# Optimization experiments

Measured on AMD Instinct MI355X. Metric: run time of the kernel, lower is better.

Reference implementation:

```python
import jax, jax.numpy as jnp
import numpy as np

N_NODES = 30000
E_EDGES = 480000
IN_DIM = 256
REL_DIM = 128
OUT_DIM = 512


def setup_inputs() -> dict:
    key = jax.random.key(0)
    ks = jax.random.split(key, 12)
    h = jax.random.normal(ks[0], (N_NODES, IN_DIM), dtype=jnp.float32)
    node_att = jax.random.uniform(ks[1], (N_NODES, 1), dtype=jnp.float32)
    rel = jax.random.normal(ks[2], (E_EDGES, REL_DIM), dtype=jnp.float32)
    edge_att = jax.random.uniform(ks[3], (E_EDGES, 1), dtype=jnp.float32)
    src = jax.random.randint(ks[4], (E_EDGES,), 0, N_NODES, dtype=jnp.int32)
    dst = jax.random.randint(ks[5], (E_EDGES,), 0, N_NODES, dtype=jnp.int32)
    # learned params (Linear: y = x @ W + b), scaled like default torch init
    def lin(k, fan_in, fan_out):
        k1, k2 = jax.random.split(k)
        bound = 1.0 / np.sqrt(fan_in)
        W = jax.random.uniform(k1, (fan_in, fan_out), minval=-bound, maxval=bound, dtype=jnp.float32)
        b = jax.random.uniform(k2, (fan_out,), minval=-bound, maxval=bound, dtype=jnp.float32)
        return W, b
    Wn, bn = lin(ks[6], IN_DIM, IN_DIM)
    Wr, br = lin(ks[7], REL_DIM, REL_DIM)
    Wa, ba = lin(ks[8], 2 * IN_DIM + REL_DIM, OUT_DIM)
    return {"h": h, "node_att": node_att, "rel": rel, "edge_att": edge_att,
            "Wn": Wn, "bn": bn, "Wr": Wr, "br": br, "Wa": Wa, "ba": ba,
            "src": src, "dst": dst}


def reference(h, node_att, rel, edge_att, Wn, bn, Wr, br, Wa, ba, src, dst):
    n_nodes = h.shape[0]
    # apply_nodes: h <- node_fc(h)  (runs BEFORE message passing)
    h2 = h @ Wn + bn                                   # [N, in]
    # message: z1 = att_src*h_src + att_dst*h_dst      [E, in]
    z1 = node_att[src] * h2[src] + node_att[dst] * h2[dst]
    # z2 = edge_att * rel_fc(rel)                      [E, rel]
    z2 = edge_att * (rel @ Wr + br)
    msg = jnp.concatenate([z1, z2], axis=1)            # [E, in+rel]
    # reduce: sum messages into destination nodes
    h_sum = jax.ops.segment_sum(msg, dst, num_segments=n_nodes)  # [N, in+rel]
    # apply_fc + relu on cat([h, h_sum])               [N, 2*in+rel] -> [N, out]
    out = jax.nn.relu(jnp.concatenate([h2, h_sum], axis=1) @ Wa + ba)
    return out
```

## Files before the change

kernel.cpp:

```cpp
#include <hip/hip_runtime.h>

#define E_EDGES 480000
#define N_NODES 30000
#define IN_DIM 256
#define REL_DIM 128
#define OUT_DIM 512
#define CAT_DIM 640
#define MTILES 1875

typedef float f32x4 __attribute__((ext_vector_type(4)));
typedef __bf16 bf16x8 __attribute__((ext_vector_type(8)));
typedef unsigned short u16x8 __attribute__((ext_vector_type(8)));

static __device__ __forceinline__ unsigned short f2bf(float x) {
    union { float f; unsigned int u; } c; c.f = x;
    unsigned int u = c.u;
    unsigned int r = u + 0x7fffu + ((u >> 16) & 1u);
    return (unsigned short)(r >> 16);
}
static __device__ __forceinline__ float bf2f(unsigned short b) {
    union { unsigned int u; float f; } c; c.u = ((unsigned int)b) << 16;
    return c.f;
}

__global__ void k_count(const int* __restrict__ dst, int* __restrict__ cnt) {
    int e = blockIdx.x * 256 + threadIdx.x;
    if (e < E_EDGES) atomicAdd(&cnt[dst[e]], 1);
}

__global__ void k_scan(const int* __restrict__ cnt, int* __restrict__ off,
                       int* __restrict__ cur) {
    __shared__ int part[1024];
    const int t = threadIdx.x;
    const int CH = (N_NODES + 1023) / 1024;
    int b = t * CH;
    int e = b + CH; if (e > N_NODES) e = N_NODES;
    if (b > N_NODES) b = N_NODES;
    int s = 0;
    for (int i = b; i < e; ++i) s += cnt[i];
    part[t] = s;
    __syncthreads();
    for (int d = 1; d < 1024; d <<= 1) {
        int v = (t >= d) ? part[t - d] : 0;
        __syncthreads();
        part[t] += v;
        __syncthreads();
    }
    int run = part[t] - s;
    for (int i = b; i < e; ++i) { off[i] = run; cur[i] = run; run += cnt[i]; }
    if (t == 1023) off[N_NODES] = run;
}

__global__ void k_fill(const int* __restrict__ dst, int* __restrict__ cur,
                       int* __restrict__ csr) {
    int e = blockIdx.x * 256 + threadIdx.x;
    if (e < E_EDGES) {
        int p = atomicAdd(&cur[dst[e]], 1);
        csr[p] = e;
    }
}

template <int K>
__launch_bounds__(256)
__global__ void gemm_small(const float* __restrict__ Ag,
                           const float* __restrict__ Bg,
                           const float* __restrict__ bias,
                           const float* __restrict__ rowb,
                           unsigned short* __restrict__ Cg,
                           int ldb, int ldc, int mtiles) {
    constexpr int KB = K / 32;
    constexpr int LDB = K + 8;
    __shared__ unsigned short Bt[64 * LDB];
    unsigned int* Bt32 = (unsigned int*)Bt;
    const int nc0 = blockIdx.y * 64;

    for (int idx = threadIdx.x; idx < 64 * (K / 2); idx += 256) {
        const int n = idx & 63;
        const int kp = idx >> 6;
        const float x0 = Bg[(size_t)(2 * kp) * ldb + nc0 + n];
        const float x1 = Bg[(size_t)(2 * kp + 1) * ldb + nc0 + n];
        Bt32[n * (LDB / 2) + kp] = (unsigned int)f2bf(x0) | ((unsigned int)f2bf(x1) << 16);
    }
    __syncthreads();

    const int lane = threadIdx.x & 63;
    const int wave = threadIdx.x >> 6;
    const int row16 = lane & 15;
    const int kgrp = lane >> 4;

    for (int mt = blockIdx.x * 4 + wave; mt < mtiles; mt += gridDim.x * 4) {
        const float* arow = Ag + (size_t)(mt * 16 + row16) * K + kgrp * 8;
        f32x4 acc[4] = {};
#pragma unroll
        for (int kb = 0; kb < KB; ++kb) {
            f32x4 a0 = *(const f32x4*)(arow + kb * 32);
            f32x4 a1 = *(const f32x4*)(arow + kb * 32 + 4);
            u16x8 au;
#pragma unroll
            for (int j = 0; j < 4; ++j) { au[j] = f2bf(a0[j]); au[4 + j] = f2bf(a1[j]); }
            bf16x8 af = __builtin_bit_cast(bf16x8, au);
#pragma unroll
            for (int nt = 0; nt < 4; ++nt) {
                bf16x8 bf = *(const bf16x8*)(&Bt[(nt * 16 + row16) * LDB + kb * 32 + kgrp * 8]);
                acc[nt] = __builtin_amdgcn_mfma_f32_16x16x32_bf16(af, bf, acc[nt], 0, 0, 0);
            }
        }
#pragma unroll
        for (int nt = 0; nt < 4; ++nt) {
            const int ocol = nc0 + nt * 16 + row16;
            const float bv = bias[ocol];
#pragma unroll
            for (int r = 0; r < 4; ++r) {
                const int orow = mt * 16 + kgrp * 4 + r;
                float v = acc[nt][r] + (rowb ? rowb[orow] * bv : bv);
                Cg[(size_t)orow * ldc + ocol] = f2bf(v);
            }
        }
    }
}

__launch_bounds__(128)
__global__ void k_gather(unsigned short* __restrict__ Amat,
                         const float* __restrict__ rel,
                         const float* __restrict__ natt,
                         const float* __restrict__ eatt,
                         const int* __restrict__ src,
                         const int* __restrict__ off,
                         const int* __restrict__ csr,
                         float* __restrict__ R,
                         float* __restrict__ S) {
    const int n = blockIdx.x;
    const int t = threadIdx.x;
    const int b = off[n], e = off[n + 1];
    float a0 = 0.f, a1 = 0.f, ar = 0.f, ae = 0.f;
    for (int i = b; i < e; ++i) {
        const int eid = csr[i];
        const int s = src[eid];
        const float w = natt[s];
        const float ea = eatt[eid];
        const unsigned int hv = *(const unsigned int*)(Amat + (size_t)s * CAT_DIM + 2 * t);
        a0 += w * bf2f((unsigned short)(hv & 0xffffu));
        a1 += w * bf2f((unsigned short)(hv >> 16));
        ar += ea * rel[(size_t)eid * REL_DIM + t];
        ae += ea;
    }
    const int deg = e - b;
    if (deg > 0) {
        const float w = (float)deg * natt[n];
        const unsigned int hv = *(const unsigned int*)(Amat + (size_t)n * CAT_DIM + 2 * t);
        a0 += w * bf2f((unsigned short)(hv & 0xffffu));
        a1 += w * bf2f((unsigned short)(hv >> 16));
    }
    const unsigned int packed = (unsigned int)f2bf(a0) | ((unsigned int)f2bf(a1) << 16);
    *(unsigned int*)(Amat + (size_t)n * CAT_DIM + IN_DIM + 2 * t) = packed;
    R[(size_t)n * REL_DIM + t] = ar;
    if (t == 0) S[n] = ae;
}

__launch_bounds__(512)
__global__ void gemm_final(const unsigned short* __restrict__ Ag,
                           const float* __restrict__ Wa,
                           const float* __restrict__ ba,
                           float* __restrict__ out) {
    constexpr int KCH = 64;
    constexpr int LDB = KCH + 8;
    __shared__ unsigned short Bt[256 * LDB];
    unsigned int* Bt32 = (unsigned int*)Bt;
    const int nc0 = blockIdx.y * 256;

    const int lane = threadIdx.x & 63;
    const int wave = threadIdx.x >> 6;
    const int row16 = lane & 15;
    const int kgrp = lane >> 4;
    const int mt = blockIdx.x * 8 + wave;
    const bool active = (mt < MTILES);

    f32x4 acc[16] = {};
    const unsigned short* arow =
        Ag + (size_t)((active ? mt : 0) * 16 + row16) * CAT_DIM + kgrp * 8;

    for (int kc = 0; kc < CAT_DIM / KCH; ++kc) {
        for (int idx = threadIdx.x; idx < 256 * (KCH / 2); idx += 512) {
            const int n = idx & 255;
            const int kp = idx >> 8;
            const int k = kc * KCH + 2 * kp;
            const float x0 = Wa[(size_t)k * OUT_DIM + nc0 + n];
            const float x1 = Wa[(size_t)(k + 1) * OUT_DIM + nc0 + n];
            Bt32[n * (LDB / 2) + kp] = (unsigned int)f2bf(x0) | ((unsigned int)f2bf(x1) << 16);
        }
        __syncthreads();
        if (active) {
#pragma unroll
            for (int kb = 0; kb < 2; ++kb) {
                bf16x8 af = __builtin_bit_cast(bf16x8,
                    *(const u16x8*)(arow + kc * KCH + kb * 32));
#pragma unroll
                for (int nt = 0; nt < 16; ++nt) {
                    bf16x8 bf = *(const bf16x8*)(&Bt[(nt * 16 + row16) * LDB + kb * 32 + kgrp * 8]);
                    acc[nt] = __builtin_amdgcn_mfma_f32_16x16x32_bf16(af, bf, acc[nt], 0, 0, 0);
                }
            }
        }
        __syncthreads();
    }
    if (active) {
#pragma unroll
        for (int nt = 0; nt < 16; ++nt) {
            const int ocol = nc0 + nt * 16 + row16;
            const float bv = ba[ocol];
#pragma unroll
            for (int r = 0; r < 4; ++r) {
                const int orow = mt * 16 + kgrp * 4 + r;
                out[(size_t)orow * OUT_DIM + ocol] = fmaxf(acc[nt][r] + bv, 0.0f);
            }
        }
    }
}

extern "C" void kernel_launch(void* const* d_in, const int* in_sizes, int n_in,
                              void* d_out, int out_size, void* d_ws, size_t ws_size,
                              hipStream_t stream) {
    const float* h    = (const float*)d_in[0];
    const float* natt = (const float*)d_in[1];
    const float* rel  = (const float*)d_in[2];
    const float* eatt = (const float*)d_in[3];
    const float* Wn   = (const float*)d_in[4];
    const float* bn   = (const float*)d_in[5];
    const float* Wr   = (const float*)d_in[6];
    const float* br   = (const float*)d_in[7];
    const float* Wa   = (const float*)d_in[8];
    const float* ba   = (const float*)d_in[9];
    const int* src    = (const int*)d_in[10];
    const int* dst    = (const int*)d_in[11];
    float* out = (float*)d_out;

    char* base = (char*)d_ws;
    unsigned short* Amat = (unsigned short*)(base);
    float* R = (float*)(base + 38400000);
    float* S = (float*)(base + 53760000);
    int* cnt = (int*)(base + 53880064);
    int* off = (int*)(base + 54000064);
    int* cur = (int*)(base + 54120128);
    int* csr = (int*)(base + 54240128);

    hipMemsetAsync(cnt, 0, N_NODES * sizeof(int), stream);
    k_count<<<(E_EDGES + 255) / 256, 256, 0, stream>>>(dst, cnt);
    k_scan<<<1, 1024, 0, stream>>>(cnt, off, cur);
    k_fill<<<(E_EDGES + 255) / 256, 256, 0, stream>>>(dst, cur, csr);

    gemm_small<256><<<dim3(469, 4), 256, 0, stream>>>(
        h, Wn, bn, nullptr, Amat, IN_DIM, CAT_DIM, MTILES);

    k_gather<<<N_NODES, 128, 0, stream>>>(Amat, rel, natt, eatt, src, off, csr, R, S);

    gemm_small<128><<<dim3(469, 2), 256, 0, stream>>>(
        R, Wr, br, S, Amat + 2 * IN_DIM, REL_DIM, CAT_DIM, MTILES);

    gemm_final<<<dim3(235, 2), 512, 0, stream>>>(Amat, Wa, ba, out);
}
```

Baseline: 669.4 us.

## Pack edge payloads into CSR, reuse A tiles across columns, double M-tiles per wave

k_fill now writes an int4 per CSR slot holding edge id, source node, edge attention and source node attention. This removes the dependent csr→src→natt/eatt loads in the gather, which is also unrolled by two edges for more memory-level parallelism. The small GEMMs now keep the converted A rows in registers and loop over all output column blocks in one 512-thread block, instead of re-reading A once per column block. gemm_final gives each wave two M-tiles so every LDS B fragment feeds two MFMAs, at the cost of higher register pressure and a larger ecp workspace.

```diff
diff --git a/kernel.cpp b/kernel.cpp
--- a/kernel.cpp
+++ b/kernel.cpp
@@ -51,69 +51,82 @@
     if (t == 1023) off[N_NODES] = run;
 }
 
-__global__ void k_fill(const int* __restrict__ dst, int* __restrict__ cur,
-                       int* __restrict__ csr) {
+__global__ void k_fill(const int* __restrict__ dst, const int* __restrict__ src,
+                       const float* __restrict__ eatt, const float* __restrict__ natt,
+                       int* __restrict__ cur, int4* __restrict__ ecp) {
     int e = blockIdx.x * 256 + threadIdx.x;
     if (e < E_EDGES) {
-        int p = atomicAdd(&cur[dst[e]], 1);
-        csr[p] = e;
-    }
-}
-
-template <int K>
-__launch_bounds__(256)
-__global__ void gemm_small(const float* __restrict__ Ag,
-                           const float* __restrict__ Bg,
-                           const float* __restrict__ bias,
-                           const float* __restrict__ rowb,
-                           unsigned short* __restrict__ Cg,
-                           int ldb, int ldc, int mtiles) {
+        const int d = dst[e];
+        const int s = src[e];
+        const int p = atomicAdd(&cur[d], 1);
+        ecp[p] = make_int4(e, s, __float_as_int(eatt[e]), __float_as_int(natt[s]));
+    }
+}
+
+template <int K, int NCOLS>
+__launch_bounds__(512)
+__global__ void gemm_As(const float* __restrict__ Ag,
+                        const float* __restrict__ Bg,
+                        const float* __restrict__ bias,
+                        const float* __restrict__ rowb,
+                        unsigned short* __restrict__ Cg,
+                        int ldc, int mtiles) {
     constexpr int KB = K / 32;
     constexpr int LDB = K + 8;
     __shared__ unsigned short Bt[64 * LDB];
     unsigned int* Bt32 = (unsigned int*)Bt;
-    const int nc0 = blockIdx.y * 64;
-
-    for (int idx = threadIdx.x; idx < 64 * (K / 2); idx += 256) {
-        const int n = idx & 63;
-        const int kp = idx >> 6;
-        const float x0 = Bg[(size_t)(2 * kp) * ldb + nc0 + n];
-        const float x1 = Bg[(size_t)(2 * kp + 1) * ldb + nc0 + n];
-        Bt32[n * (LDB / 2) + kp] = (unsigned int)f2bf(x0) | ((unsigned int)f2bf(x1) << 16);
-    }
-    __syncthreads();
 
     const int lane = threadIdx.x & 63;
     const int wave = threadIdx.x >> 6;
     const int row16 = lane & 15;
     const int kgrp = lane >> 4;
-
-    for (int mt = blockIdx.x * 4 + wave; mt < mtiles; mt += gridDim.x * 4) {
-        const float* arow = Ag + (size_t)(mt * 16 + row16) * K + kgrp * 8;
-        f32x4 acc[4] = {};
+    const int mt = blockIdx.x * 8 + wave;
+    const bool active = (mt < mtiles);
+
+    bf16x8 af[KB];
+    {
+        const float* arow = Ag + (size_t)((active ? mt : 0) * 16 + row16) * K + kgrp * 8;
 #pragma unroll
         for (int kb = 0; kb < KB; ++kb) {
-            f32x4 a0 = *(const f32x4*)(arow + kb * 32);
-            f32x4 a1 = *(const f32x4*)(arow + kb * 32 + 4);
+            f32x4 x0 = *(const f32x4*)(arow + kb * 32);
+            f32x4 x1 = *(const f32x4*)(arow + kb * 32 + 4);
             u16x8 au;
 #pragma unroll
-            for (int j = 0; j < 4; ++j) { au[j] = f2bf(a0[j]); au[4 + j] = f2bf(a1[j]); }
-            bf16x8 af = __builtin_bit_cast(bf16x8, au);
+            for (int j = 0; j < 4; ++j) { au[j] = f2bf(x0[j]); au[4 + j] = f2bf(x1[j]); }
+            af[kb] = __builtin_bit_cast(bf16x8, au);
+        }
+    }
+
+    for (int nc0 = 0; nc0 < NCOLS; nc0 += 64) {
+        __syncthreads();
+        for (int idx = threadIdx.x; idx < 64 * (K / 2); idx += 512) {
+            const int n = idx & 63;
+            const int kp = idx >> 6;
+            const float x0 = Bg[(size_t)(2 * kp) * NCOLS + nc0 + n];
+            const float x1 = Bg[(size_t)(2 * kp + 1) * NCOLS + nc0 + n];
+            Bt32[n * (LDB / 2) + kp] = (unsigned int)f2bf(x0) | ((unsigned int)f2bf(x1) << 16);
+        }
+        __syncthreads();
+        if (active) {
+            f32x4 acc[4] = {};
+#pragma unroll
+            for (int kb = 0; kb < KB; ++kb) {
+#pragma unroll
+                for (int nt = 0; nt < 4; ++nt) {
+                    bf16x8 bf = *(const bf16x8*)(&Bt[(nt * 16 + row16) * LDB + kb * 32 + kgrp * 8]);
+                    acc[nt] = __builtin_amdgcn_mfma_f32_16x16x32_bf16(af[kb], bf, acc[nt], 0, 0, 0);
+                }
+            }
 #pragma unroll
             for (int nt = 0; nt < 4; ++nt) {
-                bf16x8 bf = *(const bf16x8*)(&Bt[(nt * 16 + row16) * LDB + kb * 32 + kgrp * 8]);
-                acc[nt] = __builtin_amdgcn_mfma_f32_16x16x32_bf16(af, bf, acc[nt], 0, 0, 0);
-            }
-        }
-#pragma unroll
-        for (int nt = 0; nt < 4; ++nt) {
-            const int ocol = nc0 + nt * 16 + row16;
-            const float bv = bias[ocol];
-#pragma unroll
-            for (int r = 0; r < 4; ++r) {
-                const int orow = mt * 16 + kgrp * 4 + r;
-                float v = acc[nt][r] + (rowb ? rowb[orow] * bv : bv);
-                Cg[(size_t)orow * ldc + ocol] = f2bf(v);
+                const int ocol = nc0 + nt * 16 + row16;
+                const float bv = bias[ocol];
+#pragma unroll
+                for (int r = 0; r < 4; ++r) {
+                    const int orow = mt * 16 + kgrp * 4 + r;
+                    float v = acc[nt][r] + (rowb ? rowb[orow] * bv : bv);
+                    Cg[(size_t)orow * ldc + ocol] = f2bf(v);
+                }
             }
         }
     }
@@ -123,26 +136,38 @@
 __global__ void k_gather(unsigned short* __restrict__ Amat,
                          const float* __restrict__ rel,
                          const float* __restrict__ natt,
-                         const float* __restrict__ eatt,
-                         const int* __restrict__ src,
                          const int* __restrict__ off,
-                         const int* __restrict__ csr,
+                         const int4* __restrict__ ecp,
                          float* __restrict__ R,
                          float* __restrict__ S) {
     const int n = blockIdx.x;
     const int t = threadIdx.x;
     const int b = off[n], e = off[n + 1];
     float a0 = 0.f, a1 = 0.f, ar = 0.f, ae = 0.f;
-    for (int i = b; i < e; ++i) {
-        const int eid = csr[i];
-        const int s = src[eid];
-        const float w = natt[s];
-        const float ea = eatt[eid];
-        const unsigned int hv = *(const unsigned int*)(Amat + (size_t)s * CAT_DIM + 2 * t);
-        a0 += w * bf2f((unsigned short)(hv & 0xffffu));
-        a1 += w * bf2f((unsigned short)(hv >> 16));
-        ar += ea * rel[(size_t)eid * REL_DIM + t];
-        ae += ea;
+    int i = b;
+    for (; i + 2 <= e; i += 2) {
+        const int4 p0 = ecp[i];
+        const int4 p1 = ecp[i + 1];
+        const unsigned int hv0 = *(const unsigned int*)(Amat + (size_t)p0.y * CAT_DIM + 2 * t);
+        const float r0 = rel[(size_t)p0.x * REL_DIM + t];
+        const unsigned int hv1 = *(const unsigned int*)(Amat + (size_t)p1.y * CAT_DIM + 2 * t);
+        const float r1 = rel[(size_t)p1.x * REL_DIM + t];
+        const float ea0 = __int_as_float(p0.z), w0 = __int_as_float(p0.w);
+        const float ea1 = __int_as_float(p1.z), w1 = __int_as_float(p1.w);
+        a0 += w0 * bf2f((unsigned short)(hv0 & 0xffffu)) + w1 * bf2f((unsigned short)(hv1 & 0xffffu));
+        a1 += w0 * bf2f((unsigned short)(hv0 >> 16)) + w1 * bf2f((unsigned short)(hv1 >> 16));
+        ar += ea0 * r0 + ea1 * r1;
+        ae += ea0 + ea1;
+    }
+    if (i < e) {
+        const int4 p0 = ecp[i];
+        const unsigned int hv0 = *(const unsigned int*)(Amat + (size_t)p0.y * CAT_DIM + 2 * t);
+        const float r0 = rel[(size_t)p0.x * REL_DIM + t];
+        const float ea0 = __int_as_float(p0.z), w0 = __int_as_float(p0.w);
+        a0 += w0 * bf2f((unsigned short)(hv0 & 0xffffu));
+        a1 += w0 * bf2f((unsigned short)(hv0 >> 16));
+        ar += ea0 * r0;
+        ae += ea0;
     }
     const int deg = e - b;
     if (deg > 0) {
@@ -172,14 +197,20 @@
     const int wave = threadIdx.x >> 6;
     const int row16 = lane & 15;
     const int kgrp = lane >> 4;
-    const int mt = blockIdx.x * 8 + wave;
-    const bool active = (mt < MTILES);
-
-    f32x4 acc[16] = {};
-    const unsigned short* arow =
-        Ag + (size_t)((active ? mt : 0) * 16 + row16) * CAT_DIM + kgrp * 8;
+    const int mt0 = blockIdx.x * 16 + wave * 2;
+    const int mt1 = mt0 + 1;
+    const bool act0 = (mt0 < MTILES);
+    const bool act1 = (mt1 < MTILES);
+
+    f32x4 acc0[16] = {};
+    f32x4 acc1[16] = {};
+    const unsigned short* arow0 =
+        Ag + (size_t)((act0 ? mt0 : 0) * 16 + row16) * CAT_DIM + kgrp * 8;
+    const unsigned short* arow1 =
+        Ag + (size_t)((act1 ? mt1 : 0) * 16 + row16) * CAT_DIM + kgrp * 8;
 
     for (int kc = 0; kc < CAT_DIM / KCH; ++kc) {
+        __syncthreads();
         for (int idx = threadIdx.x; idx < 256 * (KCH / 2); idx += 512) {
             const int n = idx & 255;
             const int kp = idx >> 8;
@@ -189,29 +220,39 @@
             Bt32[n * (LDB / 2) + kp] = (unsigned int)f2bf(x0) | ((unsigned int)f2bf(x1) << 16);
         }
         __syncthreads();
-        if (active) {
-#pragma unroll
-            for (int kb = 0; kb < 2; ++kb) {
-                bf16x8 af = __builtin_bit_cast(bf16x8,
-                    *(const u16x8*)(arow + kc * KCH + kb * 32));
-#pragma unroll
-                for (int nt = 0; nt < 16; ++nt) {
-                    bf16x8 bf = *(const bf16x8*)(&Bt[(nt * 16 + row16) * LDB + kb * 32 + kgrp * 8]);
-                    acc[nt] = __builtin_amdgcn_mfma_f32_16x16x32_bf16(af, bf, acc[nt], 0, 0, 0);
-                }
-            }
-        }
-        __syncthreads();
-    }
-    if (active) {
+#pragma unroll
+        for (int kb = 0; kb < 2; ++kb) {
+            bf16x8 a0 = __builtin_bit_cast(bf16x8, *(const u16x8*)(arow0 + kc * KCH + kb * 32));
+            bf16x8 a1 = __builtin_bit_cast(bf16x8, *(const u16x8*)(arow1 + kc * KCH + kb * 32));
+#pragma unroll
+            for (int nt = 0; nt < 16; ++nt) {
+                bf16x8 bf = *(const bf16x8*)(&Bt[(nt * 16 + row16) * LDB + kb * 32 + kgrp * 8]);
+                acc0[nt] = __builtin_amdgcn_mfma_f32_16x16x32_bf16(a0, bf, acc0[nt], 0, 0, 0);
+                acc1[nt] = __builtin_amdgcn_mfma_f32_16x16x32_bf16(a1, bf, acc1[nt], 0, 0, 0);
+            }
+        }
+    }
+    if (act0) {
 #pragma unroll
         for (int nt = 0; nt < 16; ++nt) {
             const int ocol = nc0 + nt * 16 + row16;
             const float bv = ba[ocol];
 #pragma unroll
             for (int r = 0; r < 4; ++r) {
-                const int orow = mt * 16 + kgrp * 4 + r;
-                out[(size_t)orow * OUT_DIM + ocol] = fmaxf(acc[nt][r] + bv, 0.0f);
+                const int orow = mt0 * 16 + kgrp * 4 + r;
+                out[(size_t)orow * OUT_DIM + ocol] = fmaxf(acc0[nt][r] + bv, 0.0f);
+            }
+        }
+    }
+    if (act1) {
+#pragma unroll
+        for (int nt = 0; nt < 16; ++nt) {
+            const int ocol = nc0 + nt * 16 + row16;
+            const float bv = ba[ocol];
+#pragma unroll
+            for (int r = 0; r < 4; ++r) {
+                const int orow = mt1 * 16 + kgrp * 4 + r;
+                out[(size_t)orow * OUT_DIM + ocol] = fmaxf(acc1[nt][r] + bv, 0.0f);
             }
         }
     }
@@ -241,20 +282,18 @@
     int* cnt = (int*)(base + 53880064);
     int* off = (int*)(base + 54000064);
     int* cur = (int*)(base + 54120128);
-    int* csr = (int*)(base + 54240128);
+    int4* ecp = (int4*)(base + 54240128);
 
     hipMemsetAsync(cnt, 0, N_NODES * sizeof(int), stream);
     k_count<<<(E_EDGES + 255) / 256, 256, 0, stream>>>(dst, cnt);
     k_scan<<<1, 1024, 0, stream>>>(cnt, off, cur);
-    k_fill<<<(E_EDGES + 255) / 256, 256, 0, stream>>>(dst, cur, csr);
-
-    gemm_small<256><<<dim3(469, 4), 256, 0, stream>>>(
-        h, Wn, bn, nullptr, Amat, IN_DIM, CAT_DIM, MTILES);
-
-    k_gather<<<N_NODES, 128, 0, stream>>>(Amat, rel, natt, eatt, src, off, csr, R, S);
-
-    gemm_small<128><<<dim3(469, 2), 256, 0, stream>>>(
-        R, Wr, br, S, Amat + 2 * IN_DIM, REL_DIM, CAT_DIM, MTILES);
-
-    gemm_final<<<dim3(235, 2), 512, 0, stream>>>(Amat, Wa, ba, out);
-}
+    k_fill<<<(E_EDGES + 255) / 256, 256, 0, stream>>>(dst, src, eatt, natt, cur, ecp);
+
+    gemm_As<256, 256><<<235, 512, 0, stream>>>(h, Wn, bn, nullptr, Amat, CAT_DIM, MTILES);
+
+    k_gather<<<N_NODES, 128, 0, stream>>>(Amat, rel, natt, off, ecp, R, S);
+
+    gemm_As<128, 128><<<235, 512, 0, stream>>>(R, Wr, br, S, Amat + 2 * IN_DIM, CAT_DIM, MTILES);
+
+    gemm_final<<<dim3(118, 2), 512, 0, stream>>>(Amat, Wa, ba, out);
+}
```

Result: faster. 613.3 us (-8.4%).
